# Kernel optimization log

Measured on AMD Instinct MI355X. Metric: run time of the kernel, lower is better.

## Reference

```python
import jax, jax.numpy as jnp
import numpy as np

DIM = 2048
N_HEADS = 32
N_KV_HEADS = 8
HEAD_DIM = DIM // N_HEADS  # 64
ROPE_BASE = 10000
B, S = 2, 2048


def rope_cos_sin(seq_len, head_dim, base=ROPE_BASE):
    # theta: [head_dim//2]
    theta = 1.0 / (base ** (jnp.arange(0, head_dim, 2, dtype=jnp.float32) / head_dim))
    idx_theta = jnp.arange(seq_len, dtype=jnp.float32)[:, None] * theta[None, :]  # [s, hd/2]
    return jnp.cos(idx_theta), jnp.sin(idx_theta)


def apply_rope(t, cos, sin):
    # t: [b, s, h, hd]; cos/sin: [s, hd/2]
    b, s, h, hd = t.shape
    t2 = t.reshape(b, s, h, hd // 2, 2)
    x0, x1 = t2[..., 0], t2[..., 1]
    c = cos[None, :, None, :]
    sn = sin[None, :, None, :]
    out = jnp.stack([x0 * c - x1 * sn, x1 * c + x0 * sn], axis=-1)
    return out.reshape(b, s, h, hd)


def setup_inputs() -> dict:
    key = jax.random.key(0)
    k1, k2, k3 = jax.random.split(key, 3)
    x = jax.random.normal(k1, (B, S, DIM), dtype=jnp.float32)
    # packed projection weight, stored [in, out]; torch Linear would be its transpose
    packed = DIM + 2 * N_KV_HEADS * HEAD_DIM  # 3072
    w_qkv = jax.random.normal(k2, (DIM, packed), dtype=jnp.float32) * (DIM ** -0.5)
    w_out = jax.random.normal(k3, (DIM, DIM), dtype=jnp.float32) * (DIM ** -0.5)
    return {"x": x, "w_qkv": w_qkv, "w_out": w_out}


def reference(x, w_qkv, w_out):
    b, s, e = x.shape
    hd = HEAD_DIM
    kv_size = N_KV_HEADS * hd
    qkv = x @ w_qkv  # [b, s, dim + 2*kv]
    q = qkv[..., :DIM].reshape(b, s, N_HEADS, hd)
    k = qkv[..., DIM:DIM + kv_size].reshape(b, s, N_KV_HEADS, hd)
    v = qkv[..., DIM + kv_size:].reshape(b, s, N_KV_HEADS, hd)

    cos, sin = rope_cos_sin(s, hd)
    q = apply_rope(q, cos, sin)
    k = apply_rope(k, cos, sin)

    # GQA: group query heads per kv head
    g = N_HEADS // N_KV_HEADS
    q = q.transpose(0, 2, 1, 3).reshape(b, N_KV_HEADS, g, s, hd)  # [b, kh, g, s, hd]
    k = k.transpose(0, 2, 1, 3)  # [b, kh, s, hd]
    v = v.transpose(0, 2, 1, 3)

    scale = 1.0 / jnp.sqrt(jnp.float32(hd))
    scores = jnp.einsum('bkgqd,bktd->bkgqt', q, k) * scale  # [b, kh, g, s, s]
    causal = jnp.tril(jnp.ones((s, s), dtype=bool))
    scores = jnp.where(causal[None, None, None], scores, jnp.finfo(scores.dtype).min)
    probs = jax.nn.softmax(scores, axis=-1)
    attn = jnp.einsum('bkgqt,bktd->bkgqd', probs, v)  # [b, kh, g, s, hd]
    attn = attn.reshape(b, N_HEADS, s, hd).transpose(0, 2, 1, 3).reshape(b, s, DIM)
    return attn @ w_out
```

## Files before the change

kernel.cpp:

```cpp
#include <hip/hip_runtime.h>
#include <hip/hip_bf16.h>
#include <cstdint>
#include <cstddef>

#define DIME 2048
#define NH 32
#define NKV 8
#define HD 64
#define BB 2
#define SSEQ 2048
#define PACKED (DIME + 2*NKV*HD)
#define MTOT (BB*SSEQ)

typedef __attribute__((ext_vector_type(8))) short bf16x8;
typedef __attribute__((ext_vector_type(4))) float f32x4;
typedef __attribute__((ext_vector_type(16))) float f32x16;
typedef __attribute__((ext_vector_type(4))) unsigned u32x4;

__device__ __forceinline__ short f2b(float f) {
  unsigned u = __builtin_bit_cast(unsigned, f);
  u += 0x7fffu + ((u >> 16) & 1u);
  return (short)(u >> 16);
}
__device__ __forceinline__ float b2f(short s) {
  unsigned u = ((unsigned)(unsigned short)s) << 16;
  return __builtin_bit_cast(float, u);
}
__device__ __forceinline__ unsigned cvt_pk(float lo, float hi) {
  unsigned r;
  asm("v_cvt_pk_bf16_f32 %0, %1, %2" : "=v"(r) : "v"(lo), "v"(hi));
  return r;
}

__device__ __forceinline__ void gload_lds16(const void* g, void* l) {
  __builtin_amdgcn_global_load_lds(
      (const __attribute__((address_space(1))) void*)g,
      (__attribute__((address_space(3))) void*)l, 16, 0, 0);
}

__global__ __launch_bounds__(256) void cast_bf16(const float* __restrict__ in,
                                                 short* __restrict__ out, int n4) {
  int i = blockIdx.x * blockDim.x + threadIdx.x;
  int stride = gridDim.x * blockDim.x;
  for (; i < n4; i += stride) {
    float4 v = ((const float4*)in)[i];
    short4 o;
    o.x = f2b(v.x); o.y = f2b(v.y); o.z = f2b(v.z); o.w = f2b(v.w);
    ((short4*)out)[i] = o;
  }
}

__global__ __launch_bounds__(256) void transpose_cast(const float* __restrict__ in,
                                                      short* __restrict__ out,
                                                      int R, int C) {
  __shared__ float tile[32][33];
  int bx = blockIdx.x * 32;
  int by = blockIdx.y * 32;
  int tx = threadIdx.x;
  int ty = threadIdx.y;
  #pragma unroll
  for (int j = 0; j < 4; ++j)
    tile[ty + j*8][tx] = in[(size_t)(by + ty + j*8) * C + bx + tx];
  __syncthreads();
  #pragma unroll
  for (int j = 0; j < 4; ++j)
    out[(size_t)(bx + ty + j*8) * R + by + tx] = f2b(tile[tx][ty + j*8]);
}

__global__ __launch_bounds__(256) void rope_table(float* __restrict__ ctab,
                                                  float* __restrict__ stab) {
  int t = blockIdx.x * blockDim.x + threadIdx.x;
  int s = t >> 5, i = t & 31;
  float theta = 1.0f / powf(10000.0f, (float)(2 * i) * (1.0f / (float)HD));
  float ang = (float)s * theta;
  float sn, cs;
  sincosf(ang, &sn, &cs);
  ctab[t] = cs;
  stab[t] = sn;
}

__global__ __launch_bounds__(256) void gemm_bt_f32(const short* __restrict__ A,
                                                   const short* __restrict__ BT,
                                                   float* __restrict__ Cout,
                                                   int M, int N, int K) {
  __shared__ __align__(16) short lds[2][2][2][4096];
  const int tid = threadIdx.x;
  const int l = tid & 63, w = tid >> 6;
  const int lr = l & 15, lg = l >> 4;
  const int wm = w >> 1, wn = w & 1;
  const int bm = blockIdx.x * 128, bn = blockIdx.y * 128;
  const int NT = K >> 6;

  const int srow = w * 16 + (l >> 2);
  const int scol = (l & 3) * 8;

  auto stage = [&](int t, int c) {
    const int k0 = t << 6;
    #pragma unroll
    for (int s = 0; s < 2; ++s)
      #pragma unroll
      for (int j = 0; j < 2; ++j) {
        gload_lds16(A  + (size_t)(bm + j * 64 + srow) * K + k0 + s * 32 + scol,
                    &lds[c][0][s][(j * 256 + w * 64) * 8]);
        gload_lds16(BT + (size_t)(bn + j * 64 + srow) * K + k0 + s * 32 + scol,
                    &lds[c][1][s][(j * 256 + w * 64) * 8]);
      }
  };

  f32x4 acc[4][4];
  #pragma unroll
  for (int m = 0; m < 4; ++m)
    #pragma unroll
    for (int n = 0; n < 4; ++n) {
      f32x4 z = {0.f, 0.f, 0.f, 0.f};
      acc[m][n] = z;
    }

  stage(0, 0);
  stage(1, 1);
  asm volatile("s_waitcnt vmcnt(8)" ::: "memory");
  __builtin_amdgcn_sched_barrier(0);
  __builtin_amdgcn_s_barrier();

  for (int t = 0; t < NT; ++t) {
    const int c = t & 1;
    bf16x8 af[4][2], bfr[4][2];
    #pragma unroll
    for (int m = 0; m < 4; ++m)
      #pragma unroll
      for (int ks = 0; ks < 2; ++ks)
        af[m][ks] = *(const bf16x8*)&lds[c][0][ks][((wm * 64 + m * 16 + lr) * 4 + lg) * 8];
    #pragma unroll
    for (int n = 0; n < 4; ++n)
      #pragma unroll
      for (int ks = 0; ks < 2; ++ks)
        bfr[n][ks] = *(const bf16x8*)&lds[c][1][ks][((wn * 64 + n * 16 + lr) * 4 + lg) * 8];
    asm volatile("s_waitcnt lgkmcnt(0)" ::: "memory");
    __builtin_amdgcn_sched_barrier(0);
    __builtin_amdgcn_s_barrier();
    if (t + 2 < NT) stage(t + 2, c);
    __builtin_amdgcn_s_setprio(1);
    #pragma unroll
    for (int m = 0; m < 4; ++m)
      #pragma unroll
      for (int n = 0; n < 4; ++n) {
        acc[m][n] = __builtin_amdgcn_mfma_f32_16x16x32_bf16(af[m][0], bfr[n][0], acc[m][n], 0, 0, 0);
        acc[m][n] = __builtin_amdgcn_mfma_f32_16x16x32_bf16(af[m][1], bfr[n][1], acc[m][n], 0, 0, 0);
      }
    __builtin_amdgcn_s_setprio(0);
    if (t + 2 < NT) {
      asm volatile("s_waitcnt vmcnt(8)" ::: "memory");
    } else if (t + 1 < NT) {
      asm volatile("s_waitcnt vmcnt(0)" ::: "memory");
    }
    __builtin_amdgcn_sched_barrier(0);
    __builtin_amdgcn_s_barrier();
  }

  #pragma unroll
  for (int m = 0; m < 4; ++m)
    #pragma unroll
    for (int n = 0; n < 4; ++n)
      #pragma unroll
      for (int r = 0; r < 4; ++r) {
        int row = bm + wm * 64 + m * 16 + lg * 4 + r;
        int col = bn + wn * 64 + n * 16 + lr;
        Cout[(size_t)row * N + col] = acc[m][n][r];
      }
}

__global__ __launch_bounds__(256) void gemm_qkv_fused(const short* __restrict__ A,
                                                      const short* __restrict__ BT,
                                                      const float* __restrict__ ctab,
                                                      const float* __restrict__ stab,
                                                      short* __restrict__ Qo,
                                                      short* __restrict__ Ko,
                                                      short* __restrict__ VT) {
  __shared__ __align__(16) short lds[2][2][2][4096];
  const int tid = threadIdx.x;
  const int l = tid & 63, w = tid >> 6;
  const int lr = l & 15, lg = l >> 4;
  const int wm = w >> 1, wn = w & 1;
  const int bm = blockIdx.x * 128, bn = blockIdx.y * 128;
  const int K = DIME;
  const int NT = K >> 6;

  const int srow = w * 16 + (l >> 2);
  const int scol = (l & 3) * 8;

  auto stage = [&](int t, int c) {
    const int k0 = t << 6;
    #pragma unroll
    for (int s = 0; s < 2; ++s)
      #pragma unroll
      for (int j = 0; j < 2; ++j) {
        gload_lds16(A  + (size_t)(bm + j * 64 + srow) * K + k0 + s * 32 + scol,
                    &lds[c][0][s][(j * 256 + w * 64) * 8]);
        gload_lds16(BT + (size_t)(bn + j * 64 + srow) * K + k0 + s * 32 + scol,
                    &lds[c][1][s][(j * 256 + w * 64) * 8]);
      }
  };

  f32x4 acc[4][4];
  #pragma unroll
  for (int m = 0; m < 4; ++m)
    #pragma unroll
    for (int n = 0; n < 4; ++n) {
      f32x4 z = {0.f, 0.f, 0.f, 0.f};
      acc[m][n] = z;
    }

  stage(0, 0);
  stage(1, 1);
  asm volatile("s_waitcnt vmcnt(8)" ::: "memory");
  __builtin_amdgcn_sched_barrier(0);
  __builtin_amdgcn_s_barrier();

  for (int t = 0; t < NT; ++t) {
    const int c = t & 1;
    bf16x8 af[4][2], bfr[4][2];
    #pragma unroll
    for (int m = 0; m < 4; ++m)
      #pragma unroll
      for (int ks = 0; ks < 2; ++ks)
        af[m][ks] = *(const bf16x8*)&lds[c][0][ks][((wm * 64 + m * 16 + lr) * 4 + lg) * 8];
    #pragma unroll
    for (int n = 0; n < 4; ++n)
      #pragma unroll
      for (int ks = 0; ks < 2; ++ks)
        bfr[n][ks] = *(const bf16x8*)&lds[c][1][ks][((wn * 64 + n * 16 + lr) * 4 + lg) * 8];
    asm volatile("s_waitcnt lgkmcnt(0)" ::: "memory");
    __builtin_amdgcn_sched_barrier(0);
    __builtin_amdgcn_s_barrier();
    if (t + 2 < NT) stage(t + 2, c);
    __builtin_amdgcn_s_setprio(1);
    #pragma unroll
    for (int m = 0; m < 4; ++m)
      #pragma unroll
      for (int n = 0; n < 4; ++n) {
        acc[m][n] = __builtin_amdgcn_mfma_f32_16x16x32_bf16(af[m][0], bfr[n][0], acc[m][n], 0, 0, 0);
        acc[m][n] = __builtin_amdgcn_mfma_f32_16x16x32_bf16(af[m][1], bfr[n][1], acc[m][n], 0, 0, 0);
      }
    __builtin_amdgcn_s_setprio(0);
    if (t + 2 < NT) {
      asm volatile("s_waitcnt vmcnt(8)" ::: "memory");
    } else if (t + 1 < NT) {
      asm volatile("s_waitcnt vmcnt(0)" ::: "memory");
    }
    __builtin_amdgcn_sched_barrier(0);
    __builtin_amdgcn_s_barrier();
  }

  const int col0 = bn + wn * 64;
  const int rowb = bm + wm * 64;
  if (bn < DIME) {
    #pragma unroll
    for (int m = 0; m < 4; ++m)
      #pragma unroll
      for (int n = 0; n < 4; ++n) {
        const int col = col0 + n * 16 + lr;
        const int h = col >> 6, d = col & 63;
        const int ti = d >> 1;
        #pragma unroll
        for (int r = 0; r < 4; ++r) {
          const int row = rowb + m * 16 + lg * 4 + r;
          const int bb = row >> 11, s = row & 2047;
          float val = acc[m][n][r];
          float oth = __shfl_xor(val, 1);
          float cs = ctab[s * 32 + ti], snv = stab[s * 32 + ti];
          float o = (d & 1) ? (val * cs + oth * snv) : (val * cs - oth * snv);
          o *= 0.180336880f;
          Qo[((size_t)(bb * NH + h) * SSEQ + s) * HD + d] = f2b(o);
        }
      }
  } else if (bn < DIME + 512) {
    #pragma unroll
    for (int m = 0; m < 4; ++m)
      #pragma unroll
      for (int n = 0; n < 4; ++n) {
        const int col = col0 + n * 16 + lr;
        const int kvh = (col - DIME) >> 6, d = col & 63;
        const int ti = d >> 1;
        #pragma unroll
        for (int r = 0; r < 4; ++r) {
          const int row = rowb + m * 16 + lg * 4 + r;
          const int bb = row >> 11, s = row & 2047;
          float val = acc[m][n][r];
          float oth = __shfl_xor(val, 1);
          float cs = ctab[s * 32 + ti], snv = stab[s * 32 + ti];
          float o = (d & 1) ? (val * cs + oth * snv) : (val * cs - oth * snv);
          Ko[((size_t)(bb * NKV + kvh) * SSEQ + s) * HD + d] = f2b(o);
        }
      }
  } else {
    #pragma unroll
    for (int m = 0; m < 4; ++m) {
      const int row0 = rowb + m * 16 + lg * 4;
      const int bb = row0 >> 11, s = row0 & 2047;
      #pragma unroll
      for (int n = 0; n < 4; ++n) {
        const int cc = col0 - (DIME + 512) + n * 16 + lr;
        const int kvh = cc >> 6, d = cc & 63;
        short4 o4;
        o4.x = f2b(acc[m][n][0]);
        o4.y = f2b(acc[m][n][1]);
        o4.z = f2b(acc[m][n][2]);
        o4.w = f2b(acc[m][n][3]);
        *(short4*)&VT[((size_t)(bb * NKV + kvh) * HD + d) * SSEQ + s] = o4;
      }
    }
  }
}

__global__ __launch_bounds__(512) void attn_fwd(const short* __restrict__ Q,
                                                const short* __restrict__ K,
                                                const short* __restrict__ VT,
                                                short* __restrict__ Aout) {
  __shared__ __align__(16) short Ks[2][4096];
  __shared__ __align__(16) short Vs[2][4096];
  const int tid = threadIdx.x, l = tid & 63, w = tid >> 6;
  const int l31 = l & 31;
  const int hi = l >> 5;
  const int qb = 7 - (int)(blockIdx.x >> 6);
  const int bh = blockIdx.x & 63;
  const int b = bh >> 5, hh = bh & 31, kvh = hh >> 2;
  const short* Qp = Q + (size_t)(b * NH + hh) * SSEQ * HD;
  const short* Kp = K + (size_t)(b * NKV + kvh) * SSEQ * HD;
  const short* Vp = VT + (size_t)(b * NKV + kvh) * HD * SSEQ;
  const int q0 = qb * 256 + w * 32;
  const int qrow = q0 + l31;

  const int srow = tid >> 3;
  const int ssl = (tid & 7) ^ (srow & 7);
  auto stage = [&](int t, int c) {
    const int kv0s = t * 64;
    gload_lds16(Kp + (size_t)(kv0s + srow) * HD + ssl * 8, &Ks[c][w * 512]);
    gload_lds16(Vp + (size_t)srow * SSEQ + kv0s + ssl * 8, &Vs[c][w * 512]);
  };

  bf16x8 qf[4];
  #pragma unroll
  for (int ks = 0; ks < 4; ++ks)
    qf[ks] = *(const bf16x8*)&Qp[(size_t)qrow * HD + ks * 16 + hi * 8];

  f32x16 O0, O1;
  #pragma unroll
  for (int r = 0; r < 16; ++r) { O0[r] = 0.f; O1[r] = 0.f; }
  float lsum = 0.f;

  auto compute = [&](int c, int kv0) {
    bf16x8 kf0[4], kf1[4];
    #pragma unroll
    for (int ks = 0; ks < 4; ++ks) {
      kf0[ks] = *(const bf16x8*)&Ks[c][(l31 * 8 + (((ks << 1) + hi) ^ (l31 & 7))) * 8];
      kf1[ks] = *(const bf16x8*)&Ks[c][((32 + l31) * 8 + (((ks << 1) + hi) ^ (l31 & 7))) * 8];
    }
    f32x16 sacc[2];
    #pragma unroll
    for (int r = 0; r < 16; ++r) { sacc[0][r] = -20.f; sacc[1][r] = -20.f; }
    #pragma unroll
    for (int ks = 0; ks < 4; ++ks) {
      sacc[0] = __builtin_amdgcn_mfma_f32_32x32x16_bf16(kf0[ks], qf[ks], sacc[0], 0, 0, 0);
      sacc[1] = __builtin_amdgcn_mfma_f32_32x32x16_bf16(kf1[ks], qf[ks], sacc[1], 0, 0, 0);
    }
    bf16x8 vf0[4], vf1[4];
    #pragma unroll
    for (int ks = 0; ks < 4; ++ks) {
      vf0[ks] = *(const bf16x8*)&Vs[c][(l31 * 8 + (((ks << 1) + hi) ^ (l31 & 7))) * 8];
      vf1[ks] = *(const bf16x8*)&Vs[c][((32 + l31) * 8 + (((ks << 1) + hi) ^ (l31 & 7))) * 8];
    }
    if (kv0 + 63 > q0) {
      #pragma unroll
      for (int n = 0; n < 2; ++n)
        #pragma unroll
        for (int r = 0; r < 16; ++r) {
          int kvg = kv0 + n * 32 + ((r & 3) + 8 * (r >> 2)) + 4 * hi;
          if (kvg > qrow) sacc[n][r] = -3.0e38f;
        }
    }
    float ls0 = 0.f, ls1 = 0.f;
    #pragma unroll
    for (int r = 0; r < 16; ++r) {
      float e0 = exp2f(sacc[0][r]);
      float e1 = exp2f(sacc[1][r]);
      sacc[0][r] = e0;
      sacc[1][r] = e1;
      ls0 += e0;
      ls1 += e1;
    }
    lsum += ls0 + ls1;
    bf16x8 pa[4];
    #pragma unroll
    for (int n = 0; n < 2; ++n)
      #pragma unroll
      for (int s = 0; s < 2; ++s) {
        const int r0 = s * 8;
        unsigned A1 = cvt_pk(sacc[n][r0 + 0], sacc[n][r0 + 1]);
        unsigned B1 = cvt_pk(sacc[n][r0 + 4], sacc[n][r0 + 5]);
        unsigned A2 = cvt_pk(sacc[n][r0 + 2], sacc[n][r0 + 3]);
        unsigned B2 = cvt_pk(sacc[n][r0 + 6], sacc[n][r0 + 7]);
        unsigned shB1 = (unsigned)__shfl_xor((int)B1, 32);
        unsigned shA1 = (unsigned)__shfl_xor((int)A1, 32);
        unsigned shB2 = (unsigned)__shfl_xor((int)B2, 32);
        unsigned shA2 = (unsigned)__shfl_xor((int)A2, 32);
        u32x4 words;
        words[0] = hi ? shB1 : A1;
        words[1] = hi ? shB2 : A2;
        words[2] = hi ? B1 : shA1;
        words[3] = hi ? B2 : shA2;
        pa[n * 2 + s] = __builtin_bit_cast(bf16x8, words);
      }
    #pragma unroll
    for (int ks = 0; ks < 4; ++ks) {
      O0 = __builtin_amdgcn_mfma_f32_32x32x16_bf16(pa[ks], vf0[ks], O0, 0, 0, 0);
      O1 = __builtin_amdgcn_mfma_f32_32x32x16_bf16(pa[ks], vf1[ks], O1, 0, 0, 0);
    }
  };

  const int NT = (qb + 1) * 4;
  stage(0, 0);
  for (int t = 0; t < NT; ++t) {
    const int c = t & 1;
    if (t + 1 < NT) {
      stage(t + 1, c ^ 1);
      asm volatile("s_waitcnt vmcnt(2)" ::: "memory");
    } else {
      asm volatile("s_waitcnt vmcnt(0)" ::: "memory");
    }
    __builtin_amdgcn_sched_barrier(0);
    __builtin_amdgcn_s_barrier();
    const int kv0 = t * 64;
    if (kv0 <= q0 + 31) compute(c, kv0);
    __builtin_amdgcn_s_barrier();
  }

  lsum += __shfl_xor(lsum, 32);
  float inv = 1.0f / lsum;
  #pragma unroll
  for (int r = 0; r < 16; ++r) {
    int crow = (r & 3) + 8 * (r >> 2) + 4 * hi;
    float iq = __shfl(inv, crow);
    int qg = q0 + crow;
    size_t base = (size_t)(b * SSEQ + qg) * DIME + hh * HD;
    Aout[base + l31]      = f2b(O0[r] * iq);
    Aout[base + 32 + l31] = f2b(O1[r] * iq);
  }
}

extern "C" void kernel_launch(void* const* d_in, const int* in_sizes, int n_in,
                              void* d_out, int out_size, void* d_ws, size_t ws_size,
                              hipStream_t stream) {
  const float* x     = (const float*)d_in[0];
  const float* w_qkv = (const float*)d_in[1];
  const float* w_out = (const float*)d_in[2];
  float* out = (float*)d_out;

  char* ws = (char*)d_ws;
  size_t off = 0;
  auto alloc = [&](size_t bytes) -> void* {
    void* p = ws + off;
    off += (bytes + 255) & ~(size_t)255;
    return p;
  };
  short* xb    = (short*)alloc((size_t)MTOT * DIME * 2);
  short* wqkvT = (short*)alloc((size_t)PACKED * DIME * 2);
  short* woutT = (short*)alloc((size_t)DIME * DIME * 2);
  short* Qb    = (short*)alloc((size_t)BB * NH * SSEQ * HD * 2);
  short* Kb    = (short*)alloc((size_t)BB * NKV * SSEQ * HD * 2);
  short* VTb   = (short*)alloc((size_t)BB * NKV * HD * SSEQ * 2);
  short* attnb = (short*)alloc((size_t)MTOT * DIME * 2);
  float* ctab  = (float*)alloc((size_t)SSEQ * 32 * 4);
  float* stab  = (float*)alloc((size_t)SSEQ * 32 * 4);

  cast_bf16<<<2048, 256, 0, stream>>>(x, xb, MTOT * DIME / 4);
  transpose_cast<<<dim3(PACKED / 32, DIME / 32), dim3(32, 8), 0, stream>>>(w_qkv, wqkvT, DIME, PACKED);
  transpose_cast<<<dim3(DIME / 32, DIME / 32), dim3(32, 8), 0, stream>>>(w_out, woutT, DIME, DIME);
  rope_table<<<(SSEQ * 32) / 256, 256, 0, stream>>>(ctab, stab);

  gemm_qkv_fused<<<dim3(MTOT / 128, PACKED / 128), 256, 0, stream>>>(
      xb, wqkvT, ctab, stab, Qb, Kb, VTb);

  attn_fwd<<<512, 512, 0, stream>>>(Qb, Kb, VTb, attnb);

  gemm_bt_f32<<<dim3(MTOT / 128, DIME / 128), 256, 0, stream>>>(attnb, woutT, out, MTOT, DIME, DIME);
}
```

Measured before the change: 205.8 us.

## Move Q RoPE into attention load, shrink GEMM K-tile, add MFMA priority

Q's rotary embedding and softmax scale now run when attention loads Q, using a new precomputed cos/sin table that already includes the scale. The QKV GEMM epilogue stores raw Q with no shuffles or table lookups. Both GEMMs halve their K-step from 64 to 32, which halves LDS usage and doubles the loop iterations. Attention also raises wave priority around its MFMA blocks. The risks are an extra bf16 rounding of Q before RoPE and more barrier overhead per GEMM iteration.

```diff
diff --git a/kernel.cpp b/kernel.cpp
--- a/kernel.cpp
+++ b/kernel.cpp
@@ -68,7 +68,8 @@
 }
 
 __global__ __launch_bounds__(256) void rope_table(float* __restrict__ ctab,
-                                                  float* __restrict__ stab) {
+                                                  float* __restrict__ stab,
+                                                  float2* __restrict__ qtab) {
   int t = blockIdx.x * blockDim.x + threadIdx.x;
   int s = t >> 5, i = t & 31;
   float theta = 1.0f / powf(10000.0f, (float)(2 * i) * (1.0f / (float)HD));
@@ -77,34 +78,30 @@
   sincosf(ang, &sn, &cs);
   ctab[t] = cs;
   stab[t] = sn;
+  qtab[t] = make_float2(cs * 0.180336880f, sn * 0.180336880f);
 }
 
 __global__ __launch_bounds__(256) void gemm_bt_f32(const short* __restrict__ A,
                                                    const short* __restrict__ BT,
                                                    float* __restrict__ Cout,
                                                    int M, int N, int K) {
-  __shared__ __align__(16) short lds[2][2][2][4096];
+  __shared__ __align__(16) short lds[2][2][4096];
   const int tid = threadIdx.x;
   const int l = tid & 63, w = tid >> 6;
   const int lr = l & 15, lg = l >> 4;
   const int wm = w >> 1, wn = w & 1;
   const int bm = blockIdx.x * 128, bn = blockIdx.y * 128;
-  const int NT = K >> 6;
-
-  const int srow = w * 16 + (l >> 2);
-  const int scol = (l & 3) * 8;
+  const int NT = K >> 5;
 
   auto stage = [&](int t, int c) {
-    const int k0 = t << 6;
-    #pragma unroll
-    for (int s = 0; s < 2; ++s)
-      #pragma unroll
-      for (int j = 0; j < 2; ++j) {
-        gload_lds16(A  + (size_t)(bm + j * 64 + srow) * K + k0 + s * 32 + scol,
-                    &lds[c][0][s][(j * 256 + w * 64) * 8]);
-        gload_lds16(BT + (size_t)(bn + j * 64 + srow) * K + k0 + s * 32 + scol,
-                    &lds[c][1][s][(j * 256 + w * 64) * 8]);
-      }
+    const int k0 = t << 5;
+    #pragma unroll
+    for (int cc = 0; cc < 2; ++cc) {
+      const int q = cc * 256 + w * 64 + l;
+      const int row = q >> 2, col = (q & 3) * 8;
+      gload_lds16(A  + (size_t)(bm + row) * K + k0 + col, &lds[c][0][(cc * 256 + w * 64) * 8]);
+      gload_lds16(BT + (size_t)(bn + row) * K + k0 + col, &lds[c][1][(cc * 256 + w * 64) * 8]);
+    }
   };
 
   f32x4 acc[4][4];
@@ -118,23 +115,19 @@
 
   stage(0, 0);
   stage(1, 1);
-  asm volatile("s_waitcnt vmcnt(8)" ::: "memory");
+  asm volatile("s_waitcnt vmcnt(4)" ::: "memory");
   __builtin_amdgcn_sched_barrier(0);
   __builtin_amdgcn_s_barrier();
 
   for (int t = 0; t < NT; ++t) {
     const int c = t & 1;
-    bf16x8 af[4][2], bfr[4][2];
-    #pragma unroll
-    for (int m = 0; m < 4; ++m)
-      #pragma unroll
-      for (int ks = 0; ks < 2; ++ks)
-        af[m][ks] = *(const bf16x8*)&lds[c][0][ks][((wm * 64 + m * 16 + lr) * 4 + lg) * 8];
+    bf16x8 af[4], bfr[4];
+    #pragma unroll
+    for (int m = 0; m < 4; ++m)
+      af[m] = *(const bf16x8*)&lds[c][0][(wm * 64 + m * 16 + lr) * 32 + lg * 8];
     #pragma unroll
     for (int n = 0; n < 4; ++n)
-      #pragma unroll
-      for (int ks = 0; ks < 2; ++ks)
-        bfr[n][ks] = *(const bf16x8*)&lds[c][1][ks][((wn * 64 + n * 16 + lr) * 4 + lg) * 8];
+      bfr[n] = *(const bf16x8*)&lds[c][1][(wn * 64 + n * 16 + lr) * 32 + lg * 8];
     asm volatile("s_waitcnt lgkmcnt(0)" ::: "memory");
     __builtin_amdgcn_sched_barrier(0);
     __builtin_amdgcn_s_barrier();
@@ -143,13 +136,11 @@
     #pragma unroll
     for (int m = 0; m < 4; ++m)
       #pragma unroll
-      for (int n = 0; n < 4; ++n) {
-        acc[m][n] = __builtin_amdgcn_mfma_f32_16x16x32_bf16(af[m][0], bfr[n][0], acc[m][n], 0, 0, 0);
-        acc[m][n] = __builtin_amdgcn_mfma_f32_16x16x32_bf16(af[m][1], bfr[n][1], acc[m][n], 0, 0, 0);
-      }
+      for (int n = 0; n < 4; ++n)
+        acc[m][n] = __builtin_amdgcn_mfma_f32_16x16x32_bf16(af[m], bfr[n], acc[m][n], 0, 0, 0);
     __builtin_amdgcn_s_setprio(0);
     if (t + 2 < NT) {
-      asm volatile("s_waitcnt vmcnt(8)" ::: "memory");
+      asm volatile("s_waitcnt vmcnt(4)" ::: "memory");
     } else if (t + 1 < NT) {
       asm volatile("s_waitcnt vmcnt(0)" ::: "memory");
     }
@@ -176,29 +167,24 @@
                                                       short* __restrict__ Qo,
                                                       short* __restrict__ Ko,
                                                       short* __restrict__ VT) {
-  __shared__ __align__(16) short lds[2][2][2][4096];
+  __shared__ __align__(16) short lds[2][2][4096];
   const int tid = threadIdx.x;
   const int l = tid & 63, w = tid >> 6;
   const int lr = l & 15, lg = l >> 4;
   const int wm = w >> 1, wn = w & 1;
   const int bm = blockIdx.x * 128, bn = blockIdx.y * 128;
   const int K = DIME;
-  const int NT = K >> 6;
-
-  const int srow = w * 16 + (l >> 2);
-  const int scol = (l & 3) * 8;
+  const int NT = K >> 5;
 
   auto stage = [&](int t, int c) {
-    const int k0 = t << 6;
-    #pragma unroll
-    for (int s = 0; s < 2; ++s)
-      #pragma unroll
-      for (int j = 0; j < 2; ++j) {
-        gload_lds16(A  + (size_t)(bm + j * 64 + srow) * K + k0 + s * 32 + scol,
-                    &lds[c][0][s][(j * 256 + w * 64) * 8]);
-        gload_lds16(BT + (size_t)(bn + j * 64 + srow) * K + k0 + s * 32 + scol,
-                    &lds[c][1][s][(j * 256 + w * 64) * 8]);
-      }
+    const int k0 = t << 5;
+    #pragma unroll
+    for (int cc = 0; cc < 2; ++cc) {
+      const int q = cc * 256 + w * 64 + l;
+      const int row = q >> 2, col = (q & 3) * 8;
+      gload_lds16(A  + (size_t)(bm + row) * K + k0 + col, &lds[c][0][(cc * 256 + w * 64) * 8]);
+      gload_lds16(BT + (size_t)(bn + row) * K + k0 + col, &lds[c][1][(cc * 256 + w * 64) * 8]);
+    }
   };
 
   f32x4 acc[4][4];
@@ -212,23 +198,19 @@
 
   stage(0, 0);
   stage(1, 1);
-  asm volatile("s_waitcnt vmcnt(8)" ::: "memory");
+  asm volatile("s_waitcnt vmcnt(4)" ::: "memory");
   __builtin_amdgcn_sched_barrier(0);
   __builtin_amdgcn_s_barrier();
 
   for (int t = 0; t < NT; ++t) {
     const int c = t & 1;
-    bf16x8 af[4][2], bfr[4][2];
-    #pragma unroll
-    for (int m = 0; m < 4; ++m)
-      #pragma unroll
-      for (int ks = 0; ks < 2; ++ks)
-        af[m][ks] = *(const bf16x8*)&lds[c][0][ks][((wm * 64 + m * 16 + lr) * 4 + lg) * 8];
+    bf16x8 af[4], bfr[4];
+    #pragma unroll
+    for (int m = 0; m < 4; ++m)
+      af[m] = *(const bf16x8*)&lds[c][0][(wm * 64 + m * 16 + lr) * 32 + lg * 8];
     #pragma unroll
     for (int n = 0; n < 4; ++n)
-      #pragma unroll
-      for (int ks = 0; ks < 2; ++ks)
-        bfr[n][ks] = *(const bf16x8*)&lds[c][1][ks][((wn * 64 + n * 16 + lr) * 4 + lg) * 8];
+      bfr[n] = *(const bf16x8*)&lds[c][1][(wn * 64 + n * 16 + lr) * 32 + lg * 8];
     asm volatile("s_waitcnt lgkmcnt(0)" ::: "memory");
     __builtin_amdgcn_sched_barrier(0);
     __builtin_amdgcn_s_barrier();
@@ -237,13 +219,11 @@
     #pragma unroll
     for (int m = 0; m < 4; ++m)
       #pragma unroll
-      for (int n = 0; n < 4; ++n) {
-        acc[m][n] = __builtin_amdgcn_mfma_f32_16x16x32_bf16(af[m][0], bfr[n][0], acc[m][n], 0, 0, 0);
-        acc[m][n] = __builtin_amdgcn_mfma_f32_16x16x32_bf16(af[m][1], bfr[n][1], acc[m][n], 0, 0, 0);
-      }
+      for (int n = 0; n < 4; ++n)
+        acc[m][n] = __builtin_amdgcn_mfma_f32_16x16x32_bf16(af[m], bfr[n], acc[m][n], 0, 0, 0);
     __builtin_amdgcn_s_setprio(0);
     if (t + 2 < NT) {
-      asm volatile("s_waitcnt vmcnt(8)" ::: "memory");
+      asm volatile("s_waitcnt vmcnt(4)" ::: "memory");
     } else if (t + 1 < NT) {
       asm volatile("s_waitcnt vmcnt(0)" ::: "memory");
     }
@@ -260,17 +240,11 @@
       for (int n = 0; n < 4; ++n) {
         const int col = col0 + n * 16 + lr;
         const int h = col >> 6, d = col & 63;
-        const int ti = d >> 1;
         #pragma unroll
         for (int r = 0; r < 4; ++r) {
           const int row = rowb + m * 16 + lg * 4 + r;
           const int bb = row >> 11, s = row & 2047;
-          float val = acc[m][n][r];
-          float oth = __shfl_xor(val, 1);
-          float cs = ctab[s * 32 + ti], snv = stab[s * 32 + ti];
-          float o = (d & 1) ? (val * cs + oth * snv) : (val * cs - oth * snv);
-          o *= 0.180336880f;
-          Qo[((size_t)(bb * NH + h) * SSEQ + s) * HD + d] = f2b(o);
+          Qo[((size_t)(bb * NH + h) * SSEQ + s) * HD + d] = f2b(acc[m][n][r]);
         }
       }
   } else if (bn < DIME + 512) {
@@ -315,6 +289,7 @@
 __global__ __launch_bounds__(512) void attn_fwd(const short* __restrict__ Q,
                                                 const short* __restrict__ K,
                                                 const short* __restrict__ VT,
+                                                const float2* __restrict__ qtab,
                                                 short* __restrict__ Aout) {
   __shared__ __align__(16) short Ks[2][4096];
   __shared__ __align__(16) short Vs[2][4096];
@@ -339,9 +314,19 @@
   };
 
   bf16x8 qf[4];
-  #pragma unroll
-  for (int ks = 0; ks < 4; ++ks)
-    qf[ks] = *(const bf16x8*)&Qp[(size_t)qrow * HD + ks * 16 + hi * 8];
+  const float2* qt = qtab + (size_t)qrow * 32;
+  #pragma unroll
+  for (int ks = 0; ks < 4; ++ks) {
+    bf16x8 raw = *(const bf16x8*)&Qp[(size_t)qrow * HD + ks * 16 + hi * 8];
+    const int i0 = ks * 8 + hi * 4;
+    #pragma unroll
+    for (int j = 0; j < 4; ++j) {
+      float x0 = b2f(raw[2 * j]), x1 = b2f(raw[2 * j + 1]);
+      float2 cs = qt[i0 + j];
+      qf[ks][2 * j]     = f2b(x0 * cs.x - x1 * cs.y);
+      qf[ks][2 * j + 1] = f2b(x1 * cs.x + x0 * cs.y);
+    }
+  }
 
   f32x16 O0, O1;
   #pragma unroll
@@ -358,11 +343,13 @@
     f32x16 sacc[2];
     #pragma unroll
     for (int r = 0; r < 16; ++r) { sacc[0][r] = -20.f; sacc[1][r] = -20.f; }
+    __builtin_amdgcn_s_setprio(1);
     #pragma unroll
     for (int ks = 0; ks < 4; ++ks) {
       sacc[0] = __builtin_amdgcn_mfma_f32_32x32x16_bf16(kf0[ks], qf[ks], sacc[0], 0, 0, 0);
       sacc[1] = __builtin_amdgcn_mfma_f32_32x32x16_bf16(kf1[ks], qf[ks], sacc[1], 0, 0, 0);
     }
+    __builtin_amdgcn_s_setprio(0);
     bf16x8 vf0[4], vf1[4];
     #pragma unroll
     for (int ks = 0; ks < 4; ++ks) {
@@ -410,11 +397,13 @@
         words[3] = hi ? B2 : shA2;
         pa[n * 2 + s] = __builtin_bit_cast(bf16x8, words);
       }
+    __builtin_amdgcn_s_setprio(1);
     #pragma unroll
     for (int ks = 0; ks < 4; ++ks) {
       O0 = __builtin_amdgcn_mfma_f32_32x32x16_bf16(pa[ks], vf0[ks], O0, 0, 0, 0);
       O1 = __builtin_amdgcn_mfma_f32_32x32x16_bf16(pa[ks], vf1[ks], O1, 0, 0, 0);
     }
+    __builtin_amdgcn_s_setprio(0);
   };
 
   const int NT = (qb + 1) * 4;
@@ -471,16 +460,17 @@
   short* attnb = (short*)alloc((size_t)MTOT * DIME * 2);
   float* ctab  = (float*)alloc((size_t)SSEQ * 32 * 4);
   float* stab  = (float*)alloc((size_t)SSEQ * 32 * 4);
+  float2* qtab = (float2*)alloc((size_t)SSEQ * 32 * 8);
 
   cast_bf16<<<2048, 256, 0, stream>>>(x, xb, MTOT * DIME / 4);
   transpose_cast<<<dim3(PACKED / 32, DIME / 32), dim3(32, 8), 0, stream>>>(w_qkv, wqkvT, DIME, PACKED);
   transpose_cast<<<dim3(DIME / 32, DIME / 32), dim3(32, 8), 0, stream>>>(w_out, woutT, DIME, DIME);
-  rope_table<<<(SSEQ * 32) / 256, 256, 0, stream>>>(ctab, stab);
+  rope_table<<<(SSEQ * 32) / 256, 256, 0, stream>>>(ctab, stab, qtab);
 
   gemm_qkv_fused<<<dim3(MTOT / 128, PACKED / 128), 256, 0, stream>>>(
       xb, wqkvT, ctab, stab, Qb, Kb, VTb);
 
-  attn_fwd<<<512, 512, 0, stream>>>(Qb, Kb, VTb, attnb);
+  attn_fwd<<<512, 512, 0, stream>>>(Qb, Kb, VTb, qtab, attnb);
 
   gemm_bt_f32<<<dim3(MTOT / 128, DIME / 128), 256, 0, stream>>>(attnb, woutT, out, MTOT, DIME, DIME);
 }
```

Measured after the change: 217.3 us. 1.06x slower.
